# Optimization experiments

Measured on AMD Instinct MI355X. Metric: run time of the kernel, lower is better.

## Reference

```python
import jax, jax.numpy as jnp
import numpy as np

B, S, D, H = 2, 2048, 1024, 16
DK = D // H  # 64

def setup_inputs() -> dict:
    key = jax.random.key(0)
    ks = jax.random.split(key, 8)
    xavier = np.sqrt(6.0 / (D + D))  # xavier_uniform bound for square Linear
    def lin_w(k):
        return jax.random.uniform(k, (D, D), jnp.float32, -xavier, xavier)
    return {
        'Q': jax.random.normal(ks[0], (B, S, D), jnp.float32),
        'length': jax.random.randint(ks[1], (B,), 1, S + 1, jnp.int32),
        'Wq': lin_w(ks[2]), 'bq': jnp.zeros((D,), jnp.float32),
        'Wk': lin_w(ks[3]), 'bk': jnp.zeros((D,), jnp.float32),
        'Wv': lin_w(ks[4]), 'bv': jnp.zeros((D,), jnp.float32),
    }

def reference(Q, length, Wq, bq, Wk, bk, Wv, bv):
    # project and split heads: [B,S,D] -> [B,H,S,DK]
    def heads(x, W, b):
        y = jnp.einsum('bsd,de->bse', x, W) + b
        return y.reshape(B, S, H, DK).transpose(0, 2, 1, 3)
    q = heads(Q, Wq, bq)
    k = heads(Q, Wk, bk)
    v = heads(Q, Wv, bv)
    scores = jnp.einsum('bhqd,bhkd->bhqk', q, k) / np.sqrt(DK)
    scores = jnp.exp(scores)  # NOTE: raw exp, no max-subtraction (faithful)
    # multiplicative key mask: mask[b,k] = k < length[b], broadcast over q,h
    mask = (jnp.arange(S)[None, :] < length[:, None]).astype(scores.dtype)
    scores = scores * mask[:, None, None, :]
    attn = scores / (jnp.sum(scores, axis=-1, keepdims=True) + 1e-8)
    ctx = jnp.einsum('bhqk,bhkd->bhqd', attn, v)
    return ctx.transpose(0, 2, 1, 3).reshape(B, S, D)
```

## Files before the change

kernel.cpp:

```cpp
#include <hip/hip_runtime.h>
#include <hip/hip_bf16.h>

#define B_  2
#define S_  2048
#define D_  1024
#define H_  16
#define DK_ 64
#define M_  (B_ * S_)

typedef short short8 __attribute__((ext_vector_type(8)));
typedef float float4v __attribute__((ext_vector_type(4)));

#define QSCALE 0.18033688011112042f

static __device__ __forceinline__ ushort f32_to_bf16bits(float f) {
    union { __hip_bfloat16 h; ushort u; } cv;
    cv.h = __float2bfloat16(f);
    return cv.u;
}

static __device__ __forceinline__ void glds16(const ushort* g, ushort* l) {
    __builtin_amdgcn_global_load_lds(
        (const __attribute__((address_space(1))) unsigned int*)g,
        (__attribute__((address_space(3))) unsigned int*)l, 16, 0, 0);
}

__global__ __launch_bounds__(256) void prep(
    const float* __restrict__ X, const float* __restrict__ W0,
    const float* __restrict__ W1, const float* __restrict__ W2,
    ushort* __restrict__ Xb, ushort* __restrict__ Wt)
{
    const int z = blockIdx.z;
    const int t = threadIdx.x;

    if (z >= 3) {
        const int blk = (z - 3) * 256 + blockIdx.y * 16 + blockIdx.x;
        const int i = blk * 2048 + t * 8;
        float4v a = *(const float4v*)(X + i);
        float4v b = *(const float4v*)(X + i + 4);
        short8 o;
        o[0] = (short)f32_to_bf16bits(a[0]); o[1] = (short)f32_to_bf16bits(a[1]);
        o[2] = (short)f32_to_bf16bits(a[2]); o[3] = (short)f32_to_bf16bits(a[3]);
        o[4] = (short)f32_to_bf16bits(b[0]); o[5] = (short)f32_to_bf16bits(b[1]);
        o[6] = (short)f32_to_bf16bits(b[2]); o[7] = (short)f32_to_bf16bits(b[3]);
        *(short8*)(Xb + i) = o;
        return;
    }

    const float* W = (z == 0) ? W0 : ((z == 1) ? W1 : W2);
    ushort* out = Wt + (size_t)z * D_ * D_;

    __shared__ ushort tile[64 * 72];
    int n0 = blockIdx.x * 64, k0 = blockIdx.y * 64;
    int r = t >> 3, g = t & 7;

    #pragma unroll
    for (int p = 0; p < 2; ++p) {
        int rr = r + p * 32;
        const float* src = W + (size_t)(k0 + rr) * D_ + n0 + g * 8;
        float4v a = *(const float4v*)src;
        float4v b = *(const float4v*)(src + 4);
        short8 o;
        o[0] = (short)f32_to_bf16bits(a[0]); o[1] = (short)f32_to_bf16bits(a[1]);
        o[2] = (short)f32_to_bf16bits(a[2]); o[3] = (short)f32_to_bf16bits(a[3]);
        o[4] = (short)f32_to_bf16bits(b[0]); o[5] = (short)f32_to_bf16bits(b[1]);
        o[6] = (short)f32_to_bf16bits(b[2]); o[7] = (short)f32_to_bf16bits(b[3]);
        *(short8*)&tile[rr * 72 + g * 8] = o;
    }
    __syncthreads();
    #pragma unroll
    for (int p = 0; p < 2; ++p) {
        int rr = r + p * 32;
        short8 v;
        #pragma unroll
        for (int i = 0; i < 8; ++i)
            v[i] = (short)tile[(g * 8 + i) * 72 + rr];
        *(short8*)(out + (size_t)(n0 + rr) * D_ + k0 + g * 8) = v;
    }
}

__global__ __launch_bounds__(256, 2) void proj_gemm(
    const ushort* __restrict__ X,
    const ushort* __restrict__ Wt,
    const float* __restrict__ b0, const float* __restrict__ b1,
    const float* __restrict__ b2,
    const int* __restrict__ length,
    ushort* __restrict__ qkv)
{
    const int m0 = blockIdx.x * 64, n0 = blockIdx.y * 128;
    const int bidx = m0 >> 11;
    const int s0 = m0 & (S_ - 1);
    const bool kv = (s0 < length[bidx]);

    __shared__ __align__(16) ushort As[64 * 64];
    __shared__ __align__(16) ushort Bs[3][128 * 64];

    const int t = threadIdx.x;
    const int lane = t & 63, wid = t >> 6;
    const int quad = lane >> 4, l16 = lane & 15;
    const int wr = wid >> 1, wc = wid & 1;

    float4v accq[2][4] = {}, acck[2][4] = {}, accv[2][4] = {};

    for (int kt = 0; kt < 16; ++kt) {
        const int k0 = kt * 64;
        __syncthreads();
        #pragma unroll
        for (int j = 0; j < 2; ++j) {
            const int cid = wid * 128 + j * 64 + lane;
            const int row = cid >> 3;
            const int cl  = (cid & 7) ^ (row & 7);
            glds16(X + (size_t)(m0 + row) * D_ + k0 + cl * 8, &As[cid * 8]);
        }
        #pragma unroll
        for (int j = 0; j < 4; ++j) {
            const int cid = wid * 256 + j * 64 + lane;
            const int row = cid >> 3;
            const int cl  = (cid & 7) ^ (row & 7);
            const size_t off = (size_t)(n0 + row) * D_ + k0 + cl * 8;
            glds16(Wt + off, &Bs[0][cid * 8]);
            if (kv) {
                glds16(Wt + (size_t)D_ * D_ + off,     &Bs[1][cid * 8]);
                glds16(Wt + (size_t)2 * D_ * D_ + off, &Bs[2][cid * 8]);
            }
        }
        __syncthreads();

        #pragma unroll
        for (int ks = 0; ks < 2; ++ks) {
            short8 a[2];
            #pragma unroll
            for (int i = 0; i < 2; ++i) {
                const int r = wr * 32 + i * 16 + l16;
                const int ph = (ks * 4 + quad) ^ (r & 7);
                a[i] = *(short8*)&As[r * 64 + ph * 8];
            }
            short8 bq[4];
            #pragma unroll
            for (int j = 0; j < 4; ++j) {
                const int r = wc * 64 + j * 16 + l16;
                const int ph = (ks * 4 + quad) ^ (r & 7);
                bq[j] = *(short8*)&Bs[0][r * 64 + ph * 8];
            }
            #pragma unroll
            for (int i = 0; i < 2; ++i)
                #pragma unroll
                for (int j = 0; j < 4; ++j)
                    accq[i][j] = __builtin_amdgcn_mfma_f32_16x16x32_bf16(
                        a[i], bq[j], accq[i][j], 0, 0, 0);
            if (kv) {
                short8 bk[4], bv[4];
                #pragma unroll
                for (int j = 0; j < 4; ++j) {
                    const int r = wc * 64 + j * 16 + l16;
                    const int ph = (ks * 4 + quad) ^ (r & 7);
                    bk[j] = *(short8*)&Bs[1][r * 64 + ph * 8];
                    bv[j] = *(short8*)&Bs[2][r * 64 + ph * 8];
                }
                #pragma unroll
                for (int i = 0; i < 2; ++i)
                    #pragma unroll
                    for (int j = 0; j < 4; ++j) {
                        acck[i][j] = __builtin_amdgcn_mfma_f32_16x16x32_bf16(
                            a[i], bk[j], acck[i][j], 0, 0, 0);
                        accv[i][j] = __builtin_amdgcn_mfma_f32_16x16x32_bf16(
                            a[i], bv[j], accv[i][j], 0, 0, 0);
                    }
            }
        }
    }

    #pragma unroll
    for (int j = 0; j < 4; ++j) {
        const int col = n0 + wc * 64 + j * 16 + l16;
        const int h = col >> 6, dk = col & (DK_ - 1);
        const float bvq = b0[col], bvk = b1[col], bvv = b2[col];
        #pragma unroll
        for (int i = 0; i < 2; ++i) {
            #pragma unroll
            for (int rr = 0; rr < 4; ++rr) {
                const int row = m0 + wr * 32 + i * 16 + quad * 4 + rr;
                const int s = row & (S_ - 1);
                const size_t hdr = ((size_t)(bidx * H_ + h) * S_ + s) * DK_ + dk;
                qkv[hdr] = f32_to_bf16bits((accq[i][j][rr] + bvq) * QSCALE);
                if (kv) {
                    qkv[(size_t)M_ * D_ + hdr] =
                        f32_to_bf16bits(acck[i][j][rr] + bvk);
                    qkv[(size_t)2 * M_ * D_ +
                        ((size_t)(bidx * H_ + h) * DK_ + dk) * S_ + s] =
                        f32_to_bf16bits(accv[i][j][rr] + bvv);
                }
            }
        }
    }
}

__global__ __launch_bounds__(256, 4) void attention(
    const ushort* __restrict__ qkv, const int* __restrict__ length,
    float* __restrict__ out)
{
    const int bid  = blockIdx.x;
    const int work = (bid & 7) * 128 + (bid >> 3);
    const int q0 = (work & 31) * 64;
    const int bh = work >> 5;
    const int b  = bh & 1;
    const int h  = bh >> 1;

    int len = length[b];
    if (len > S_) len = S_;
    if (len < 1) len = 1;
    const int nkt = (len + 63) >> 6;

    const ushort* qb = qkv + ((size_t)(b * H_ + h) * S_ + q0) * DK_;
    const ushort* kb = qkv + (size_t)M_ * D_ + (size_t)(b * H_ + h) * S_ * DK_;
    const ushort* vb = qkv + (size_t)2 * M_ * D_ + (size_t)(b * H_ + h) * DK_ * S_;

    __shared__ __align__(16) ushort QPs[64 * 64];
    __shared__ __align__(16) ushort Ks[2][64 * 64];
    __shared__ __align__(16) ushort Vs[2][64 * 64];

    const int t = threadIdx.x, lane = t & 63, wid = t >> 6;
    const int quad = lane >> 4, l16 = lane & 15;
    const int qrow = wid * 16 + l16;
    const int e8 = (l16 & 7) << 1;

    #pragma unroll
    for (int j = 0; j < 2; ++j) {
        const int cid = wid * 128 + j * 64 + lane;
        const int row = cid >> 3;
        const int cl  = (cid & 7) ^ (row & 7);
        glds16(qb + (size_t)row * DK_ + cl * 8, &QPs[cid * 8]);
        glds16(kb + (size_t)row * DK_ + cl * 8, &Ks[0][cid * 8]);
        glds16(vb + (size_t)row * S_ + cl * 8,  &Vs[0][cid * 8]);
    }
    __syncthreads();

    short8 qfrag[2];
    #pragma unroll
    for (int ks = 0; ks < 2; ++ks) {
        const int phb = (ks * 4 + quad) ^ (l16 & 7);
        qfrag[ks] = *(short8*)&QPs[qrow * 64 + phb * 8];
    }

    short8 ones8;
    #pragma unroll
    for (int i = 0; i < 8; ++i) ones8[i] = (short)0x3F80;

    float4v cacc[4] = {};
    float4v racc = {};

    for (int kt = 0; kt < nkt; ++kt) {
        const int cur = kt & 1, nxt = cur ^ 1;
        if (kt + 1 < nkt) {
            #pragma unroll
            for (int j = 0; j < 2; ++j) {
                const int cid = wid * 128 + j * 64 + lane;
                const int row = cid >> 3;
                const int cl  = (cid & 7) ^ (row & 7);
                glds16(kb + (size_t)((kt + 1) * 64 + row) * DK_ + cl * 8,
                       &Ks[nxt][cid * 8]);
                glds16(vb + (size_t)row * S_ + (kt + 1) * 64 + cl * 8,
                       &Vs[nxt][cid * 8]);
            }
        }

        float4v sacc[4] = {};
        #pragma unroll
        for (int ks = 0; ks < 2; ++ks) {
            #pragma unroll
            for (int ct = 0; ct < 4; ++ct) {
                const int krow = ct * 16 + l16;
                const int pha = (ks * 4 + quad) ^ (krow & 7);
                short8 ak = *(short8*)&Ks[cur][krow * 64 + pha * 8];
                sacc[ct] = __builtin_amdgcn_mfma_f32_16x16x32_bf16(
                    ak, qfrag[ks], sacc[ct], 0, 0, 0);
            }
        }

        const bool full = ((kt + 1) * 64 <= len);
        #pragma unroll
        for (int ct = 0; ct < 4; ++ct) {
            float v0 = __builtin_amdgcn_exp2f(sacc[ct][0]);
            float v1 = __builtin_amdgcn_exp2f(sacc[ct][1]);
            float v2 = __builtin_amdgcn_exp2f(sacc[ct][2]);
            float v3 = __builtin_amdgcn_exp2f(sacc[ct][3]);
            if (!full) {
                const int kb0 = kt * 64 + ct * 16 + quad * 4;
                v0 = (kb0 + 0 < len) ? v0 : 0.f;
                v1 = (kb0 + 1 < len) ? v1 : 0.f;
                v2 = (kb0 + 2 < len) ? v2 : 0.f;
                v3 = (kb0 + 3 < len) ? v3 : 0.f;
            }
            uint2 w;
            w.x = (__float_as_uint(v0) >> 16) | (__float_as_uint(v1) & 0xFFFF0000u);
            w.y = (__float_as_uint(v2) >> 16) | (__float_as_uint(v3) & 0xFFFF0000u);
            const int c8 = (ct * 4 + quad) ^ e8;
            *(uint2*)&QPs[qrow * 64 + c8 * 4] = w;
        }

        #pragma unroll
        for (int ks = 0; ks < 2; ++ks) {
            const int pp = ((ks * 4 + quad) * 2) ^ e8;
            short8 ap = *(short8*)&QPs[qrow * 64 + pp * 4];
            #pragma unroll
            for (int ct = 0; ct < 4; ++ct) {
                const int vrow = ct * 16 + l16;
                const int phv = (ks * 4 + quad) ^ (vrow & 7);
                short8 vv = *(short8*)&Vs[cur][vrow * 64 + phv * 8];
                cacc[ct] = __builtin_amdgcn_mfma_f32_16x16x32_bf16(
                    ap, vv, cacc[ct], 0, 0, 0);
            }
            racc = __builtin_amdgcn_mfma_f32_16x16x32_bf16(
                ap, ones8, racc, 0, 0, 0);
        }
        __syncthreads();
    }

    #pragma unroll
    for (int rr = 0; rr < 4; ++rr) {
        const float inv = 1.0f / (racc[rr] + 1e-8f);
        const int q = q0 + wid * 16 + quad * 4 + rr;
        #pragma unroll
        for (int ct = 0; ct < 4; ++ct) {
            const int d = h * 64 + ct * 16 + l16;
            out[((size_t)b * S_ + q) * D_ + d] = cacc[ct][rr] * inv;
        }
    }
}

extern "C" void kernel_launch(void* const* d_in, const int* in_sizes, int n_in,
                              void* d_out, int out_size, void* d_ws, size_t ws_size,
                              hipStream_t stream)
{
    const float* Q   = (const float*)d_in[0];
    const int*   len = (const int*)d_in[1];
    const float* Wq  = (const float*)d_in[2];
    const float* bq  = (const float*)d_in[3];
    const float* Wk  = (const float*)d_in[4];
    const float* bk  = (const float*)d_in[5];
    const float* Wv  = (const float*)d_in[6];
    const float* bv  = (const float*)d_in[7];
    float* out = (float*)d_out;

    ushort* ws  = (ushort*)d_ws;
    ushort* Xb  = ws;
    ushort* Wt  = ws + (size_t)M_ * D_;
    ushort* qkv = Wt + (size_t)3 * D_ * D_;

    dim3 gPr(16, 16, 11);
    prep<<<gPr, 256, 0, stream>>>(Q, Wq, Wk, Wv, Xb, Wt);

    dim3 gP(M_ / 64, D_ / 128);
    proj_gemm<<<gP, 256, 0, stream>>>(Xb, Wt, bq, bk, bv, len, qkv);

    attention<<<dim3(S_ / 64 * H_ * B_), 256, 0, stream>>>(qkv, len, out);
}
```

Baseline: 157.4 us.

## Keep attention probabilities in registers via permuted K-row mapping, drop LDS round-trip

Permutes which K rows each lane reads in the QK^T MFMA so that the output score fragments line up directly with the A-operand layout of the PV MFMA. The exp'd probabilities are packed to bf16 in registers instead of being written to and re-read from shared memory. Q fragments are loaded directly from global memory instead of through LDS, and the K swizzle is changed to match the new row mapping. This removes the LDS write/read and the shared Q buffer, at the cost of more complex index math and uncoalesced direct Q loads.

```diff
diff --git a/kernel.cpp b/kernel.cpp
--- a/kernel.cpp
+++ b/kernel.cpp
@@ -215,32 +215,32 @@
     const ushort* kb = qkv + (size_t)M_ * D_ + (size_t)(b * H_ + h) * S_ * DK_;
     const ushort* vb = qkv + (size_t)2 * M_ * D_ + (size_t)(b * H_ + h) * DK_ * S_;
 
-    __shared__ __align__(16) ushort QPs[64 * 64];
     __shared__ __align__(16) ushort Ks[2][64 * 64];
     __shared__ __align__(16) ushort Vs[2][64 * 64];
 
     const int t = threadIdx.x, lane = t & 63, wid = t >> 6;
     const int quad = lane >> 4, l16 = lane & 15;
-    const int qrow = wid * 16 + l16;
-    const int e8 = (l16 & 7) << 1;
+
+    const int klocal = ((l16 >> 2) << 3) + (l16 & 3);
+    const int hk     = (l16 & 3) | (((l16 >> 2) & 1) << 2);
+
+    short8 qfrag[2];
+    {
+        const ushort* qp = qb + (size_t)(wid * 16 + l16) * DK_;
+        qfrag[0] = *(const short8*)(qp + quad * 8);
+        qfrag[1] = *(const short8*)(qp + (4 + quad) * 8);
+    }
 
     #pragma unroll
     for (int j = 0; j < 2; ++j) {
         const int cid = wid * 128 + j * 64 + lane;
         const int row = cid >> 3;
-        const int cl  = (cid & 7) ^ (row & 7);
-        glds16(qb + (size_t)row * DK_ + cl * 8, &QPs[cid * 8]);
-        glds16(kb + (size_t)row * DK_ + cl * 8, &Ks[0][cid * 8]);
-        glds16(vb + (size_t)row * S_ + cl * 8,  &Vs[0][cid * 8]);
+        const int c   = cid & 7;
+        const int hKr = (row & 3) | (((row >> 3) & 1) << 2);
+        glds16(kb + (size_t)row * DK_ + (c ^ hKr) * 8, &Ks[0][cid * 8]);
+        glds16(vb + (size_t)row * S_ + (c ^ (row & 7)) * 8, &Vs[0][cid * 8]);
     }
     __syncthreads();
-
-    short8 qfrag[2];
-    #pragma unroll
-    for (int ks = 0; ks < 2; ++ks) {
-        const int phb = (ks * 4 + quad) ^ (l16 & 7);
-        qfrag[ks] = *(short8*)&QPs[qrow * 64 + phb * 8];
-    }
 
     short8 ones8;
     #pragma unroll
@@ -256,10 +256,11 @@
             for (int j = 0; j < 2; ++j) {
                 const int cid = wid * 128 + j * 64 + lane;
                 const int row = cid >> 3;
-                const int cl  = (cid & 7) ^ (row & 7);
-                glds16(kb + (size_t)((kt + 1) * 64 + row) * DK_ + cl * 8,
+                const int c   = cid & 7;
+                const int hKr = (row & 3) | (((row >> 3) & 1) << 2);
+                glds16(kb + (size_t)((kt + 1) * 64 + row) * DK_ + (c ^ hKr) * 8,
                        &Ks[nxt][cid * 8]);
-                glds16(vb + (size_t)row * S_ + (kt + 1) * 64 + cl * 8,
+                glds16(vb + (size_t)row * S_ + (kt + 1) * 64 + (c ^ (row & 7)) * 8,
                        &Vs[nxt][cid * 8]);
             }
         }
@@ -269,8 +270,8 @@
         for (int ks = 0; ks < 2; ++ks) {
             #pragma unroll
             for (int ct = 0; ct < 4; ++ct) {
-                const int krow = ct * 16 + l16;
-                const int pha = (ks * 4 + quad) ^ (krow & 7);
+                const int krow = ((ct >> 1) << 5) + ((ct & 1) << 2) + klocal;
+                const int pha = (ks * 4 + quad) ^ hk;
                 short8 ak = *(short8*)&Ks[cur][krow * 64 + pha * 8];
                 sacc[ct] = __builtin_amdgcn_mfma_f32_16x16x32_bf16(
                     ak, qfrag[ks], sacc[ct], 0, 0, 0);
@@ -278,40 +279,44 @@
         }
 
         const bool full = ((kt + 1) * 64 <= len);
-        #pragma unroll
-        for (int ct = 0; ct < 4; ++ct) {
-            float v0 = __builtin_amdgcn_exp2f(sacc[ct][0]);
-            float v1 = __builtin_amdgcn_exp2f(sacc[ct][1]);
-            float v2 = __builtin_amdgcn_exp2f(sacc[ct][2]);
-            float v3 = __builtin_amdgcn_exp2f(sacc[ct][3]);
-            if (!full) {
-                const int kb0 = kt * 64 + ct * 16 + quad * 4;
-                v0 = (kb0 + 0 < len) ? v0 : 0.f;
-                v1 = (kb0 + 1 < len) ? v1 : 0.f;
-                v2 = (kb0 + 2 < len) ? v2 : 0.f;
-                v3 = (kb0 + 3 < len) ? v3 : 0.f;
-            }
-            uint2 w;
-            w.x = (__float_as_uint(v0) >> 16) | (__float_as_uint(v1) & 0xFFFF0000u);
-            w.y = (__float_as_uint(v2) >> 16) | (__float_as_uint(v3) & 0xFFFF0000u);
-            const int c8 = (ct * 4 + quad) ^ e8;
-            *(uint2*)&QPs[qrow * 64 + c8 * 4] = w;
-        }
-
+        short8 ap[2];
         #pragma unroll
         for (int ks = 0; ks < 2; ++ks) {
-            const int pp = ((ks * 4 + quad) * 2) ^ e8;
-            short8 ap = *(short8*)&QPs[qrow * 64 + pp * 4];
+            union { uint u[4]; short8 s; } cv;
+            #pragma unroll
+            for (int hh = 0; hh < 2; ++hh) {
+                const int ct = 2 * ks + hh;
+                float e0 = __builtin_amdgcn_exp2f(sacc[ct][0]);
+                float e1 = __builtin_amdgcn_exp2f(sacc[ct][1]);
+                float e2 = __builtin_amdgcn_exp2f(sacc[ct][2]);
+                float e3 = __builtin_amdgcn_exp2f(sacc[ct][3]);
+                if (!full) {
+                    const int kb0 = kt * 64 + ks * 32 + quad * 8 + hh * 4;
+                    e0 = (kb0 + 0 < len) ? e0 : 0.f;
+                    e1 = (kb0 + 1 < len) ? e1 : 0.f;
+                    e2 = (kb0 + 2 < len) ? e2 : 0.f;
+                    e3 = (kb0 + 3 < len) ? e3 : 0.f;
+                }
+                cv.u[hh * 2 + 0] = (__float_as_uint(e0) >> 16) |
+                                   (__float_as_uint(e1) & 0xFFFF0000u);
+                cv.u[hh * 2 + 1] = (__float_as_uint(e2) >> 16) |
+                                   (__float_as_uint(e3) & 0xFFFF0000u);
+            }
+            ap[ks] = cv.s;
+        }
+
+        #pragma unroll
+        for (int ks = 0; ks < 2; ++ks) {
             #pragma unroll
             for (int ct = 0; ct < 4; ++ct) {
                 const int vrow = ct * 16 + l16;
                 const int phv = (ks * 4 + quad) ^ (vrow & 7);
                 short8 vv = *(short8*)&Vs[cur][vrow * 64 + phv * 8];
                 cacc[ct] = __builtin_amdgcn_mfma_f32_16x16x32_bf16(
-                    ap, vv, cacc[ct], 0, 0, 0);
+                    ap[ks], vv, cacc[ct], 0, 0, 0);
             }
             racc = __builtin_amdgcn_mfma_f32_16x16x32_bf16(
-                ap, ones8, racc, 0, 0, 0);
+                ap[ks], ones8, racc, 0, 0, 0);
         }
         __syncthreads();
     }
```

Result: faster. 154.0 us (-2.2%).
